# Optimization experiments

Measured on AMD Instinct MI355X. Metric: run time of the kernel, lower is better.

Reference implementation:

```python
import jax, jax.numpy as jnp
import numpy as np

B, TE, TD, HE, HD = 8, 256, 128, 512, 512


def setup_inputs() -> dict:
    key = jax.random.key(0)
    k1, k2, k3, k4, k5 = jax.random.split(key, 5)
    # scale weights down (original uses 'uniform' init) to keep tanh unsaturated
    return {
        "encoder_out_seq": jax.random.normal(k1, (B, TE, HE), dtype=jnp.float32),
        "decoder_out_seq": jax.random.normal(k2, (B, TD, HD), dtype=jnp.float32),
        "W_a": jax.random.normal(k3, (HE, HE), dtype=jnp.float32) * 0.05,
        "U_a": jax.random.normal(k4, (HD, HE), dtype=jnp.float32) * 0.05,
        "V_a": jax.random.normal(k5, (HE, 1), dtype=jnp.float32) * 0.05,
    }


def reference(encoder_out_seq, decoder_out_seq, W_a, U_a, V_a):
    # Bahdanau additive attention, vectorized over all decoder timesteps
    # (the original loops over Td via K.rnn; steps are independent).
    Ws = jnp.einsum('bte,eh->bth', encoder_out_seq, W_a)   # [B, Te, He]
    Uh = jnp.einsum('bdk,kh->bdh', decoder_out_seq, U_a)   # [B, Td, He]
    # tanh(S.Wa + h.Ua): broadcast to [B, Td, Te, He], contract with V_a
    act = jnp.tanh(Ws[:, None, :, :] + Uh[:, :, None, :])  # [B, Td, Te, He]
    e = jnp.einsum('bdth,ho->bdt', act, V_a)                # [B, Td, Te]
    e = jax.nn.softmax(e, axis=-1)                          # attention weights
    c = jnp.einsum('bdt,bth->bdh', e, encoder_out_seq)      # [B, Td, He] contexts
    return (c, e)
```

## Files before the change

kernel.cpp:

```cpp
#include <hip/hip_runtime.h>

#define B_  8
#define TE_ 256
#define TD_ 128
#define HE_ 512

typedef __attribute__((ext_vector_type(4))) short short4v;
typedef __attribute__((ext_vector_type(8))) short short8v;
typedef __attribute__((ext_vector_type(4))) float f32x4;

__device__ __forceinline__ unsigned short f2bf(float x) {
  union { float f; unsigned u; } v; v.f = x;
  unsigned r = v.u + 0x7fff + ((v.u >> 16) & 1);
  return (unsigned short)(r >> 16);
}
__device__ __forceinline__ float bf2f(unsigned short b) {
  union { float f; unsigned u; } v; v.u = ((unsigned)b) << 16;
  return v.f;
}

#define GBAR() asm volatile("s_waitcnt lgkmcnt(0)\n\ts_barrier" ::: "memory")

__global__ __launch_bounds__(256) void conv_all(
    const float* __restrict__ enc, const float* __restrict__ dec,
    const float* __restrict__ Wa, const float* __restrict__ Ua,
    short* __restrict__ Ahi, short* __restrict__ Alo,
    short* __restrict__ BWhi, short* __restrict__ BWlo,
    short* __restrict__ BUhi, short* __restrict__ BUlo) {
  __shared__ float sT[64][68];
  int bid = blockIdx.x;
  const int tid = threadIdx.x;
  if (bid < 1536) {
    int idx = bid * 256 + tid;
    const int m = idx >> 7;
    const int k = (idx & 127) << 2;
    const float* src = (m < 2048) ? (enc + (size_t)m * 512 + k)
                                  : (dec + (size_t)(m - 2048) * 512 + k);
    float4 v = *(const float4*)src;
    float vf[4] = {v.x, v.y, v.z, v.w};
    short4v hi, lo;
    for (int j = 0; j < 4; ++j) {
      unsigned short h = f2bf(vf[j]);
      hi[j] = (short)h;
      lo[j] = (short)f2bf(vf[j] - bf2f(h));
    }
    *(short4v*)(Ahi + (size_t)m * 512 + k) = hi;
    *(short4v*)(Alo + (size_t)m * 512 + k) = lo;
    return;
  }
  bid -= 1536;
  const float* src; short *dhi, *dlo;
  if (bid < 64) { src = Wa; dhi = BWhi; dlo = BWlo; }
  else          { bid -= 64; src = Ua; dhi = BUhi; dlo = BUlo; }
  const int kt = (bid >> 3) * 64, nt = (bid & 7) * 64;
  const int lr = tid >> 4;
  const int lc = (tid & 15) * 4;
  for (int i = 0; i < 4; ++i) {
    float4 v = *(const float4*)(src + (size_t)(kt + lr + i * 16) * 512 + nt + lc);
    sT[lr + i * 16][lc + 0] = v.x;
    sT[lr + i * 16][lc + 1] = v.y;
    sT[lr + i * 16][lc + 2] = v.z;
    sT[lr + i * 16][lc + 3] = v.w;
  }
  __syncthreads();
  const int n_l = tid >> 2;
  const int kq  = (tid & 3) * 16;
  short8v h0v, h1v, l0v, l1v;
  for (int j = 0; j < 8; ++j) {
    float x0 = sT[kq + j][n_l];
    float x1 = sT[kq + 8 + j][n_l];
    unsigned short h0 = f2bf(x0), h1 = f2bf(x1);
    h0v[j] = (short)h0; l0v[j] = (short)f2bf(x0 - bf2f(h0));
    h1v[j] = (short)h1; l1v[j] = (short)f2bf(x1 - bf2f(h1));
  }
  size_t base = (size_t)(nt + n_l) * 512 + kt + kq;
  *(short8v*)(dhi + base)     = h0v;
  *(short8v*)(dhi + base + 8) = h1v;
  *(short8v*)(dlo + base)     = l0v;
  *(short8v*)(dlo + base + 8) = l1v;
}

__global__ __launch_bounds__(256) void gemm_mfma(
    const short* __restrict__ Ahi, const short* __restrict__ Alo,
    const short* __restrict__ BWhi, const short* __restrict__ BWlo,
    const short* __restrict__ BUhi, const short* __restrict__ BUlo,
    float* __restrict__ C) {
  __shared__ short sAh[2][128][40];
  __shared__ short sAl[2][128][40];
  __shared__ short sBh[2][64][40];
  __shared__ short sBl[2][64][40];
  const int bid = blockIdx.x;
  const int mt = bid % 24, nt = bid / 24;
  const short *Bhp, *Blp;
  if (mt < 16) { Bhp = BWhi; Blp = BWlo; }
  else         { Bhp = BUhi; Blp = BUlo; }
  const int m0 = mt * 128;
  const int n0 = nt * 64;
  const int tid = threadIdx.x;
  const int arow = tid >> 1, ak = (tid & 1) * 16;
  const int brow = tid >> 2, bk = (tid & 3) * 8;
  const int wave = tid >> 6, lane = tid & 63;
  const int wr = (wave >> 1) * 64, wc = (wave & 1) * 32;
  const int fm = lane & 15, fk = (lane >> 4) * 8;
  const int r0 = (lane >> 4) * 4, ccol = lane & 15;
  f32x4 acc[4][2] = {};
  const short* Aph = Ahi + (size_t)(m0 + arow) * 512 + ak;
  const short* Apl = Alo + (size_t)(m0 + arow) * 512 + ak;
  const short* Bph = Bhp + (size_t)(n0 + brow) * 512 + bk;
  const short* Bpl = Blp + (size_t)(n0 + brow) * 512 + bk;
  short8v rah0, rah1, ral0, ral1, rbh, rbl;
#define LOAD6(KO) { \
    rah0 = *(const short8v*)(Aph + (KO)); \
    rah1 = *(const short8v*)(Aph + (KO) + 8); \
    ral0 = *(const short8v*)(Apl + (KO)); \
    ral1 = *(const short8v*)(Apl + (KO) + 8); \
    rbh  = *(const short8v*)(Bph + (KO)); \
    rbl  = *(const short8v*)(Bpl + (KO)); }
#define STORE6(P) { \
    *(short8v*)&sAh[P][arow][ak]     = rah0; \
    *(short8v*)&sAh[P][arow][ak + 8] = rah1; \
    *(short8v*)&sAl[P][arow][ak]     = ral0; \
    *(short8v*)&sAl[P][arow][ak + 8] = ral1; \
    *(short8v*)&sBh[P][brow][bk]     = rbh; \
    *(short8v*)&sBl[P][brow][bk]     = rbl; }
  LOAD6(0);
  STORE6(0);
  LOAD6(32);
  __syncthreads();
  int p = 0;
  for (int it = 0; it < 16; ++it) {
    short8v ah[4], al[4], bh2[2], bl2[2];
#pragma unroll
    for (int i = 0; i < 4; ++i) ah[i] = *(const short8v*)&sAh[p][wr + i * 16 + fm][fk];
#pragma unroll
    for (int j = 0; j < 2; ++j) {
      bh2[j] = *(const short8v*)&sBh[p][wc + j * 16 + fm][fk];
      bl2[j] = *(const short8v*)&sBl[p][wc + j * 16 + fm][fk];
    }
#pragma unroll
    for (int i = 0; i < 4; ++i)
#pragma unroll
      for (int j = 0; j < 2; ++j)
        acc[i][j] = __builtin_amdgcn_mfma_f32_16x16x32_bf16(ah[i], bh2[j], acc[i][j], 0, 0, 0);
#pragma unroll
    for (int i = 0; i < 4; ++i)
#pragma unroll
      for (int j = 0; j < 2; ++j)
        acc[i][j] = __builtin_amdgcn_mfma_f32_16x16x32_bf16(ah[i], bl2[j], acc[i][j], 0, 0, 0);
#pragma unroll
    for (int i = 0; i < 4; ++i) al[i] = *(const short8v*)&sAl[p][wr + i * 16 + fm][fk];
#pragma unroll
    for (int i = 0; i < 4; ++i)
#pragma unroll
      for (int j = 0; j < 2; ++j)
        acc[i][j] = __builtin_amdgcn_mfma_f32_16x16x32_bf16(al[i], bh2[j], acc[i][j], 0, 0, 0);
    if (it < 15) STORE6(1 - p);
    if (it < 14) LOAD6((it + 2) * 32);
    GBAR();
    p ^= 1;
  }
#pragma unroll
  for (int i = 0; i < 4; ++i)
#pragma unroll
    for (int j = 0; j < 2; ++j) {
      const int row = m0 + wr + i * 16 + r0;
      const int col = n0 + wc + j * 16 + ccol;
#pragma unroll
      for (int r = 0; r < 4; ++r)
        C[(size_t)(row + r) * 512 + col] = acc[i][j][r];
    }
}

#define C2 2.8853900817779268f
__global__ __launch_bounds__(512) void attn_fused(
    const float* __restrict__ Ws, const float* __restrict__ Uh,
    const float* __restrict__ Va, const float* __restrict__ enc,
    float* __restrict__ c_out, float* __restrict__ e_out) {
  __shared__ float sUh[2][HE_];
  __shared__ float sV[HE_];
  __shared__ float sE[2][TE_];
  __shared__ float sRed[8];
  __shared__ float sNorm[2];
  const int tid = threadIdx.x;
  const int b  = blockIdx.x & 7;
  const int d0 = (blockIdx.x >> 3) * 2;
  if (tid < 256)
    ((float4*)sUh)[tid] = ((const float4*)(Uh + (size_t)(b * TD_ + d0) * HE_))[tid];
  else if (tid < 384)
    ((float4*)sV)[tid - 256] = ((const float4*)Va)[tid - 256];
  __syncthreads();
  const int lane = tid & 63, wave = tid >> 6;
  const int tb = wave << 5;
  const int h0 = lane << 3;
  float uhc0[8], uhc1[8], vv2[8], sumv = 0.f;
#pragma unroll
  for (int j = 0; j < 8; ++j) {
    const float vj = sV[h0 + j];
    sumv += vj;
    vv2[j] = 2.0f * vj;
    uhc0[j] = C2 * sUh[0][h0 + j];
    uhc1[j] = C2 * sUh[1][h0 + j];
  }
  const float* pw = Ws + (size_t)b * TE_ * HE_ + (size_t)tb * HE_ + h0;
  float4 a0 = *(const float4*)(pw);
  float4 a1 = *(const float4*)(pw + 4);
#define TELT2(W, J) { \
    float g0 = fmaf(C2, (W), uhc0[J]); \
    float g1 = fmaf(C2, (W), uhc1[J]); \
    float E0 = __builtin_amdgcn_exp2f(g0); \
    float E1 = __builtin_amdgcn_exp2f(g1); \
    float r0 = __builtin_amdgcn_rcpf(E0 + 1.0f); \
    float r1 = __builtin_amdgcn_rcpf(E1 + 1.0f); \
    s0 = fmaf(-vv2[J], r0, s0); \
    s1 = fmaf(-vv2[J], r1, s1); }
  for (int ti = 0; ti < 32; ++ti) {
    const float* pn = pw + HE_;
    float4 n0 = *(const float4*)(pn);
    float4 n1 = *(const float4*)(pn + 4);
    float s0 = sumv, s1 = sumv;
    TELT2(a0.x, 0)
    TELT2(a0.y, 1)
    TELT2(a0.z, 2)
    TELT2(a0.w, 3)
    TELT2(a1.x, 4)
    TELT2(a1.y, 5)
    TELT2(a1.z, 6)
    TELT2(a1.w, 7)
#pragma unroll
    for (int off = 32; off; off >>= 1) {
      s0 += __shfl_down(s0, off, 64);
      s1 += __shfl_down(s1, off, 64);
    }
    if (lane == 0) { sE[0][tb + ti] = s0; sE[1][tb + ti] = s1; }
    a0 = n0; a1 = n1;
    pw = pn;
  }
  __syncthreads();
  const int d = tid >> 8, t = tid & 255;
  const float ex = __expf(sE[d][t]);
  float sum = ex;
#pragma unroll
  for (int off = 32; off; off >>= 1) sum += __shfl_down(sum, off, 64);
  if (lane == 0) sRed[wave] = sum;
  __syncthreads();
  if (tid < 2)
    sNorm[tid] = 1.0f / (sRed[tid * 4] + sRed[tid * 4 + 1] + sRed[tid * 4 + 2] + sRed[tid * 4 + 3]);
  __syncthreads();
  const float wgt = ex * sNorm[d];
  sE[d][t] = wgt;
  e_out[(size_t)(b * TD_ + d0 + d) * TE_ + t] = wgt;
  __syncthreads();
  float a0c = 0.f, a1c = 0.f;
  const float* ep = enc + (size_t)b * TE_ * HE_ + tid;
#pragma unroll 4
  for (int tt = 0; tt < TE_; ++tt) {
    const float ev = ep[(size_t)tt * HE_];
    a0c = fmaf(sE[0][tt], ev, a0c);
    a1c = fmaf(sE[1][tt], ev, a1c);
  }
  float* cp = c_out + (size_t)(b * TD_ + d0) * HE_ + tid;
  cp[0]   = a0c;
  cp[HE_] = a1c;
}

extern "C" void kernel_launch(void* const* d_in, const int* in_sizes, int n_in,
                              void* d_out, int out_size, void* d_ws, size_t ws_size,
                              hipStream_t stream) {
  const float* enc = (const float*)d_in[0];
  const float* dec = (const float*)d_in[1];
  const float* Wa  = (const float*)d_in[2];
  const float* Ua  = (const float*)d_in[3];
  const float* Va  = (const float*)d_in[4];
  float* c_out = (float*)d_out;
  float* e_out = c_out + (size_t)B_ * TD_ * HE_;
  char* ws = (char*)d_ws;
  float* Cws  = (float*)(ws);
  short* Ahi  = (short*)(ws + (6u << 20));
  short* Alo  = (short*)(ws + (9u << 20));
  short* BWhi = (short*)(ws + (12u << 20));
  short* BWlo = (short*)(ws + (12u << 20) + (1u << 19));
  short* BUhi = (short*)(ws + (13u << 20));
  short* BUlo = (short*)(ws + (13u << 20) + (1u << 19));
  const float* Ws = Cws;
  const float* Uh = Cws + (size_t)2048 * 512;
  conv_all<<<1664, 256, 0, stream>>>(enc, dec, Wa, Ua, Ahi, Alo, BWhi, BWlo, BUhi, BUlo);
  gemm_mfma<<<192, 256, 0, stream>>>(Ahi, Alo, BWhi, BWlo, BUhi, BUlo, Cws);
  attn_fused<<<512, 512, 0, stream>>>(Ws, Uh, Va, enc, c_out, e_out);
}
```

Measured before the change: 127.8 us.

## Stage GEMM tiles via direct global-to-LDS loads with XOR-swizzled layout

Rewrites the split-bf16 GEMM mainloop to use global_load_lds so tiles go straight from global memory into shared memory without passing through registers. The LDS layout becomes an XOR-swizzled 64-element-K tile, which halves the number of loop iterations and is meant to avoid bank conflicts. Synchronisation now relies on vmcnt waits and barriers around a double buffer. The aim is to cut register pressure and the load/store staging overhead, at the cost of more fragile manual synchronisation. A macro variable rename in the attention kernel only avoids a name clash.

```diff
diff --git a/kernel.cpp b/kernel.cpp
--- a/kernel.cpp
+++ b/kernel.cpp
@@ -18,8 +18,6 @@
   union { float f; unsigned u; } v; v.u = ((unsigned)b) << 16;
   return v.f;
 }
-
-#define GBAR() asm volatile("s_waitcnt lgkmcnt(0)\n\ts_barrier" ::: "memory")
 
 __global__ __launch_bounds__(256) void conv_all(
     const float* __restrict__ enc, const float* __restrict__ dec,
@@ -80,84 +78,87 @@
   *(short8v*)(dlo + base + 8) = l1v;
 }
 
+#define S_PER_BUF 24576
 __global__ __launch_bounds__(256) void gemm_mfma(
     const short* __restrict__ Ahi, const short* __restrict__ Alo,
     const short* __restrict__ BWhi, const short* __restrict__ BWlo,
     const short* __restrict__ BUhi, const short* __restrict__ BUlo,
     float* __restrict__ C) {
-  __shared__ short sAh[2][128][40];
-  __shared__ short sAl[2][128][40];
-  __shared__ short sBh[2][64][40];
-  __shared__ short sBl[2][64][40];
+  __shared__ __align__(16) short S[2 * S_PER_BUF];
   const int bid = blockIdx.x;
   const int mt = bid % 24, nt = bid / 24;
-  const short *Bhp, *Blp;
-  if (mt < 16) { Bhp = BWhi; Blp = BWlo; }
-  else         { Bhp = BUhi; Blp = BUlo; }
-  const int m0 = mt * 128;
-  const int n0 = nt * 64;
-  const int tid = threadIdx.x;
-  const int arow = tid >> 1, ak = (tid & 1) * 16;
-  const int brow = tid >> 2, bk = (tid & 3) * 8;
-  const int wave = tid >> 6, lane = tid & 63;
-  const int wr = (wave >> 1) * 64, wc = (wave & 1) * 32;
-  const int fm = lane & 15, fk = (lane >> 4) * 8;
-  const int r0 = (lane >> 4) * 4, ccol = lane & 15;
+  const short* Bhp = (mt < 16) ? BWhi : BUhi;
+  const short* Blp = (mt < 16) ? BWlo : BUlo;
+  const int m0 = mt * 128, n0 = nt * 64;
+  const int tid = threadIdx.x, w = tid >> 6, lane = tid & 63;
+  const int laneoff = ((lane >> 3) << 10) + ((((lane & 7) ^ ((lane >> 3) & 7))) << 4);
+  const char* gsrc[12]; int loff[12];
+#pragma unroll
+  for (int q = 0; q < 12; ++q) {
+    const int v = w * 12 + q;
+    const char* base; int vj, toff;
+    if (v < 16)      { base = (const char*)(Ahi + (size_t)m0 * 512); vj = v;      toff = 0; }
+    else if (v < 32) { base = (const char*)(Alo + (size_t)m0 * 512); vj = v - 16; toff = 8192; }
+    else if (v < 40) { base = (const char*)(Bhp + (size_t)n0 * 512); vj = v - 32; toff = 16384; }
+    else             { base = (const char*)(Blp + (size_t)n0 * 512); vj = v - 40; toff = 20480; }
+    gsrc[q] = base + (size_t)vj * 8192 + laneoff;
+    loff[q] = toff + vj * 512;
+  }
+#define ISSUE(IT, P) { const int koff_ = (IT) * 128; \
+    _Pragma("unroll") \
+    for (int q = 0; q < 12; ++q) \
+      __builtin_amdgcn_global_load_lds(gsrc[q] + koff_, &S[(P) * S_PER_BUF + loff[q]], 16, 0, 0); }
+  const int wr = (w >> 1) * 64, wc = (w & 1) * 32;
+  const int fm = lane & 15, fchunk = lane >> 4;
+  const int r0 = fchunk * 4, ccol = fm;
   f32x4 acc[4][2] = {};
-  const short* Aph = Ahi + (size_t)(m0 + arow) * 512 + ak;
-  const short* Apl = Alo + (size_t)(m0 + arow) * 512 + ak;
-  const short* Bph = Bhp + (size_t)(n0 + brow) * 512 + bk;
-  const short* Bpl = Blp + (size_t)(n0 + brow) * 512 + bk;
-  short8v rah0, rah1, ral0, ral1, rbh, rbl;
-#define LOAD6(KO) { \
-    rah0 = *(const short8v*)(Aph + (KO)); \
-    rah1 = *(const short8v*)(Aph + (KO) + 8); \
-    ral0 = *(const short8v*)(Apl + (KO)); \
-    ral1 = *(const short8v*)(Apl + (KO) + 8); \
-    rbh  = *(const short8v*)(Bph + (KO)); \
-    rbl  = *(const short8v*)(Bpl + (KO)); }
-#define STORE6(P) { \
-    *(short8v*)&sAh[P][arow][ak]     = rah0; \
-    *(short8v*)&sAh[P][arow][ak + 8] = rah1; \
-    *(short8v*)&sAl[P][arow][ak]     = ral0; \
-    *(short8v*)&sAl[P][arow][ak + 8] = ral1; \
-    *(short8v*)&sBh[P][brow][bk]     = rbh; \
-    *(short8v*)&sBl[P][brow][bk]     = rbl; }
-  LOAD6(0);
-  STORE6(0);
-  LOAD6(32);
-  __syncthreads();
-  int p = 0;
-  for (int it = 0; it < 16; ++it) {
-    short8v ah[4], al[4], bh2[2], bl2[2];
-#pragma unroll
-    for (int i = 0; i < 4; ++i) ah[i] = *(const short8v*)&sAh[p][wr + i * 16 + fm][fk];
-#pragma unroll
-    for (int j = 0; j < 2; ++j) {
-      bh2[j] = *(const short8v*)&sBh[p][wc + j * 16 + fm][fk];
-      bl2[j] = *(const short8v*)&sBl[p][wc + j * 16 + fm][fk];
-    }
-#pragma unroll
-    for (int i = 0; i < 4; ++i)
-#pragma unroll
-      for (int j = 0; j < 2; ++j)
-        acc[i][j] = __builtin_amdgcn_mfma_f32_16x16x32_bf16(ah[i], bh2[j], acc[i][j], 0, 0, 0);
-#pragma unroll
-    for (int i = 0; i < 4; ++i)
-#pragma unroll
-      for (int j = 0; j < 2; ++j)
-        acc[i][j] = __builtin_amdgcn_mfma_f32_16x16x32_bf16(ah[i], bl2[j], acc[i][j], 0, 0, 0);
-#pragma unroll
-    for (int i = 0; i < 4; ++i) al[i] = *(const short8v*)&sAl[p][wr + i * 16 + fm][fk];
-#pragma unroll
-    for (int i = 0; i < 4; ++i)
-#pragma unroll
-      for (int j = 0; j < 2; ++j)
-        acc[i][j] = __builtin_amdgcn_mfma_f32_16x16x32_bf16(al[i], bh2[j], acc[i][j], 0, 0, 0);
-    if (it < 15) STORE6(1 - p);
-    if (it < 14) LOAD6((it + 2) * 32);
-    GBAR();
-    p ^= 1;
+  ISSUE(0, 0);
+  ISSUE(1, 1);
+  asm volatile("s_waitcnt vmcnt(12)\n\ts_barrier" ::: "memory");
+  for (int it = 0; it < 8; ++it) {
+    const int p = it & 1;
+    const short* Sb = &S[p * S_PER_BUF];
+#pragma unroll
+    for (int s = 0; s < 2; ++s) {
+      short8v ah[4], al[4], bh[2], bl[2];
+      const int cc = s * 4 + fchunk;
+#pragma unroll
+      for (int i = 0; i < 4; ++i) {
+        const int m = wr + i * 16 + fm;
+        const int a16 = m * 8 + (cc ^ (m & 7));
+        ah[i] = *(const short8v*)&Sb[a16 * 8];
+        al[i] = *(const short8v*)&Sb[8192 + a16 * 8];
+      }
+#pragma unroll
+      for (int j = 0; j < 2; ++j) {
+        const int n = wc + j * 16 + fm;
+        const int b16 = n * 8 + (cc ^ (n & 7));
+        bh[j] = *(const short8v*)&Sb[16384 + b16 * 8];
+        bl[j] = *(const short8v*)&Sb[20480 + b16 * 8];
+      }
+#pragma unroll
+      for (int i = 0; i < 4; ++i)
+#pragma unroll
+        for (int j = 0; j < 2; ++j)
+          acc[i][j] = __builtin_amdgcn_mfma_f32_16x16x32_bf16(ah[i], bh[j], acc[i][j], 0, 0, 0);
+#pragma unroll
+      for (int i = 0; i < 4; ++i)
+#pragma unroll
+        for (int j = 0; j < 2; ++j)
+          acc[i][j] = __builtin_amdgcn_mfma_f32_16x16x32_bf16(ah[i], bl[j], acc[i][j], 0, 0, 0);
+#pragma unroll
+      for (int i = 0; i < 4; ++i)
+#pragma unroll
+        for (int j = 0; j < 2; ++j)
+          acc[i][j] = __builtin_amdgcn_mfma_f32_16x16x32_bf16(al[i], bh[j], acc[i][j], 0, 0, 0);
+    }
+    if (it < 6) {
+      asm volatile("s_barrier" ::: "memory");
+      ISSUE(it + 2, p);
+      asm volatile("s_waitcnt vmcnt(12)\n\ts_barrier" ::: "memory");
+    } else if (it == 6) {
+      asm volatile("s_waitcnt vmcnt(0)\n\ts_barrier" ::: "memory");
+    }
   }
 #pragma unroll
   for (int i = 0; i < 4; ++i)
@@ -169,6 +170,7 @@
       for (int r = 0; r < 4; ++r)
         C[(size_t)(row + r) * 512 + col] = acc[i][j][r];
     }
+#undef ISSUE
 }
 
 #define C2 2.8853900817779268f
@@ -209,10 +211,10 @@
     float g1 = fmaf(C2, (W), uhc1[J]); \
     float E0 = __builtin_amdgcn_exp2f(g0); \
     float E1 = __builtin_amdgcn_exp2f(g1); \
-    float r0 = __builtin_amdgcn_rcpf(E0 + 1.0f); \
-    float r1 = __builtin_amdgcn_rcpf(E1 + 1.0f); \
-    s0 = fmaf(-vv2[J], r0, s0); \
-    s1 = fmaf(-vv2[J], r1, s1); }
+    float r0_ = __builtin_amdgcn_rcpf(E0 + 1.0f); \
+    float r1_ = __builtin_amdgcn_rcpf(E1 + 1.0f); \
+    s0 = fmaf(-vv2[J], r0_, s0); \
+    s1 = fmaf(-vv2[J], r1_, s1); }
   for (int ti = 0; ti < 32; ++ti) {
     const float* pn = pw + HE_;
     float4 n0 = *(const float4*)(pn);
```

Result: faster. 123.9 us (-3.0%).
